# Performance work log

Measured on AMD Instinct MI355X. Metric: run time of the kernel, lower is better.

The kernel has to match this reference:

```python
import jax, jax.numpy as jnp
import numpy as np
import math

B, T, C = 2, 2048, 1024
H, DK, DV = 16, 64, 64


def setup_inputs() -> dict:
    key = jax.random.key(0)
    ks = jax.random.split(key, 5)
    # randw(*d) = randn(*d) / sqrt(d[-1])
    x = jax.random.normal(ks[0], (B, T, C), dtype=jnp.float32)
    w_q = jax.random.normal(ks[1], (H, DK, C), dtype=jnp.float32) / math.sqrt(C)
    w_k = jax.random.normal(ks[2], (H, DK, C), dtype=jnp.float32) / math.sqrt(C)
    w_v = jax.random.normal(ks[3], (H, DV, C), dtype=jnp.float32) / math.sqrt(C)
    w_o = jax.random.normal(ks[4], (H * DV, C), dtype=jnp.float32) / math.sqrt(C)
    return {"x": x, "w_q": w_q, "w_k": w_k, "w_v": w_v, "w_o": w_o}


def reference(x, w_q, w_k, w_v, w_o):
    # Full prefill: bs_q.first = 0, bs_q.nb = T, causal=True, dropout=0 (eval).
    dk = w_q.shape[1]
    q = jnp.einsum('ntc,hdc->nhtd', x, w_q)  # [B,H,T,DK]
    k = jnp.einsum('ntc,hdc->nhtd', x, w_k)  # [B,H,T,DK]
    v = jnp.einsum('ntc,hdc->nhtd', x, w_v)  # [B,H,T,DV]
    a = jnp.einsum('nhtd,nhsd->nhts', q, k) / jnp.sqrt(jnp.asarray(dk, x.dtype))
    # amm_generator: mask where query_idx < key_idx (strict upper triangle)
    t = a.shape[-1]
    mask = jnp.arange(t)[:, None] < jnp.arange(t)[None, :]  # [T,T] bool
    a = jnp.where(mask[None, None], jnp.asarray(-jnp.inf, a.dtype), a)
    a = jax.nn.softmax(a, axis=-1)
    y = jnp.einsum('nhts,nhsd->nthd', a, v)  # [B,T,H,DV]
    y = y.reshape(y.shape[0], y.shape[1], -1)  # [B,T,H*DV]
    return y @ w_o  # [B,T,C]
```

## Files before the change

kernel.cpp:

```cpp
#include <hip/hip_runtime.h>
#include <hip/hip_bf16.h>

#define B_ 2
#define T_ 2048
#define C_ 1024
#define H_ 16
#define D_ 64

typedef __attribute__((ext_vector_type(8))) short bf16x8;
typedef __attribute__((ext_vector_type(4))) float f32x4;
typedef __attribute__((ext_vector_type(8))) unsigned short u16x8;
typedef __attribute__((ext_vector_type(2))) unsigned int u32x2;
typedef __attribute__((ext_vector_type(4))) unsigned int u32x4;

__device__ __forceinline__ unsigned short bf1(float a) {
    __bf16 x = (__bf16)a;
    return __builtin_bit_cast(unsigned short, x);
}
__device__ __forceinline__ unsigned int pk2(float a, float b) {
    return (unsigned int)bf1(a) | ((unsigned int)bf1(b) << 16);
}

__device__ __forceinline__ void gll16(const void* g, void* l) {
    __builtin_amdgcn_global_load_lds(
        (const __attribute__((address_space(1))) unsigned int*)g,
        (__attribute__((address_space(3))) unsigned int*)l, 16, 0, 0);
}

__global__ __launch_bounds__(256) void prep_x(
    const float* __restrict__ x, unsigned short* __restrict__ xb)
{
    const size_t i = ((size_t)blockIdx.x * 256 + threadIdx.x) * 16;
    float4 f0 = *reinterpret_cast<const float4*>(x + i);
    float4 f1 = *reinterpret_cast<const float4*>(x + i + 4);
    float4 f2 = *reinterpret_cast<const float4*>(x + i + 8);
    float4 f3 = *reinterpret_cast<const float4*>(x + i + 12);
    u32x4 a = {pk2(f0.x, f0.y), pk2(f0.z, f0.w), pk2(f1.x, f1.y), pk2(f1.z, f1.w)};
    u32x4 b = {pk2(f2.x, f2.y), pk2(f2.z, f2.w), pk2(f3.x, f3.y), pk2(f3.z, f3.w)};
    *reinterpret_cast<u32x4*>(xb + i) = a;
    *reinterpret_cast<u32x4*>(xb + i + 8) = b;
}

__global__ __launch_bounds__(256) void prep_w(
    const float* __restrict__ wq, const float* __restrict__ wk,
    const float* __restrict__ wv, unsigned short* __restrict__ wb)
{
    const int bid = blockIdx.x, tid = threadIdx.x;
    const int rb = bid * 4;
    const float* src = (rb < 1024) ? wq + (size_t)rb * 1024
                     : (rb < 2048) ? wk + (size_t)(rb - 1024) * 1024
                                   : wv + (size_t)(rb - 2048) * 1024;
    const float sc = (rb < 1024) ? 0.125f * 1.4426950408889634f : 1.0f;
    const float4* s4 = (const float4*)src;
    u32x2* d = (u32x2*)(wb + (size_t)rb * 1024);
#pragma unroll
    for (int k = 0; k < 4; k++) {
        float4 v = s4[k * 256 + tid];
        u32x2 w;
        w[0] = pk2(v.x * sc, v.y * sc);
        w[1] = pk2(v.z * sc, v.w * sc);
        d[k * 256 + tid] = w;
    }
}

__global__ __launch_bounds__(256) void prep_wo(
    const float* __restrict__ wo, unsigned short* __restrict__ wt)
{
    __shared__ unsigned short tile[64][72];
    const int tk = (blockIdx.x & 15) << 6, tn = (blockIdx.x >> 4) << 6;
    const int r = threadIdx.x >> 2, cb = (threadIdx.x & 3) << 4;
#pragma unroll
    for (int j = 0; j < 4; j++) {
        float4 v = *reinterpret_cast<const float4*>(
            wo + (size_t)(tk + r) * 1024 + tn + cb + j * 4);
        u32x2 w;
        w[0] = pk2(v.x, v.y);
        w[1] = pk2(v.z, v.w);
        *reinterpret_cast<u32x2*>(&tile[r][cb + j * 4]) = w;
    }
    __syncthreads();
    unsigned short buf[16];
#pragma unroll
    for (int j = 0; j < 16; j++) buf[j] = tile[cb + j][r];
    unsigned short* dst = wt + (size_t)(tn + r) * 1024 + tk + cb;
    *reinterpret_cast<u16x8*>(dst) = *reinterpret_cast<u16x8*>(buf);
    *reinterpret_cast<u16x8*>(dst + 8) = *reinterpret_cast<u16x8*>(buf + 8);
}

__global__ __launch_bounds__(256) void qkv_gemm(
    const unsigned short* __restrict__ xb, const unsigned short* __restrict__ wb,
    unsigned short* __restrict__ qkv)
{
    __shared__ __align__(16) unsigned short As[2][128 * 64];
    __shared__ __align__(16) unsigned short Bs[2][128 * 64];
    const int tid = threadIdx.x;
    const int lane = tid & 63, wave = tid >> 6;
    const int g = lane >> 4, c16 = lane & 15;
    const int xcd = blockIdx.x & 7, idx = blockIdx.x >> 3;
    const int bm = (xcd << 2) + idx / 24, bn = idx % 24;
    const int jbase = bn << 7;
    const int which = jbase >> 10;

    const int srow = wave * 32 + (lane >> 3);
    const int swc = ((lane & 7) ^ (lane >> 3)) << 3;
    const unsigned short* asrc = xb + ((size_t)(bm << 7) + srow) * C_ + swc;
    const unsigned short* bsrc = wb + ((size_t)(bn << 7) + srow) * C_ + swc;

    f32x4 acc[4][4];
#pragma unroll
    for (int i = 0; i < 4; i++)
#pragma unroll
        for (int j = 0; j < 4; j++) acc[i][j] = (f32x4){0.f, 0.f, 0.f, 0.f};

    const int wm = (wave >> 1) << 6, wn = (wave & 1) << 6;

    auto stage = [&](int buf, int k0) {
#pragma unroll
        for (int i = 0; i < 4; i++) {
            gll16(asrc + k0 + i * 8 * C_, &As[buf][(wave * 32 + i * 8) << 6]);
            gll16(bsrc + k0 + i * 8 * C_, &Bs[buf][(wave * 32 + i * 8) << 6]);
        }
    };

    stage(0, 0);
    int cur = 0;
    for (int t = 0; t < 16; ++t) {
        __syncthreads();
        if (t < 15) stage(cur ^ 1, (t + 1) << 6);
#pragma unroll
        for (int kk = 0; kk < 2; kk++) {
            bf16x8 af[4], bfv[4];
#pragma unroll
            for (int m = 0; m < 4; m++)
                af[m] = *reinterpret_cast<const bf16x8*>(
                    &As[cur][((wm + m * 16 + c16) << 6) + ((((kk << 2) + g) ^ (c16 & 7)) << 3)]);
#pragma unroll
            for (int n = 0; n < 4; n++)
                bfv[n] = *reinterpret_cast<const bf16x8*>(
                    &Bs[cur][((wn + n * 16 + c16) << 6) + ((((kk << 2) + g) ^ (c16 & 7)) << 3)]);
#pragma unroll
            for (int m = 0; m < 4; m++)
#pragma unroll
                for (int n = 0; n < 4; n++)
                    acc[m][n] = __builtin_amdgcn_mfma_f32_16x16x32_bf16(af[m], bfv[n], acc[m][n], 0, 0, 0);
        }
        cur ^= 1;
    }

    if (which < 2) {
#pragma unroll
        for (int m = 0; m < 4; m++) {
            const int grow = (bm << 7) + wm + m * 16 + (g << 2);
#pragma unroll
            for (int n = 0; n < 4; n++) {
                const int jj = (jbase + wn + n * 16 + c16) & 1023;
                const int h = jj >> 6, d = jj & 63;
#pragma unroll
                for (int r = 0; r < 4; r++) {
                    const int row = grow + r;
                    const int b = row >> 11, t = row & 2047;
                    const size_t off = ((size_t)((which * B_ + b) * H_ + h) * T_ + t) * 64 + d;
                    qkv[off] = bf1(acc[m][n][r]);
                }
            }
        }
    } else {
#pragma unroll
        for (int m = 0; m < 4; m++) {
            const int grow = (bm << 7) + wm + m * 16 + (g << 2);
            const int b = grow >> 11, t = grow & 2047;
#pragma unroll
            for (int n = 0; n < 4; n++) {
                const int jj = (jbase + wn + n * 16 + c16) & 1023;
                const int h = jj >> 6, d = jj & 63;
                u32x2 w;
                w[0] = pk2(acc[m][n][0], acc[m][n][1]);
                w[1] = pk2(acc[m][n][2], acc[m][n][3]);
                const size_t off = ((size_t)((2 * B_ + b) * H_ + h) * 64 + d) * T_ + t;
                *reinterpret_cast<u32x2*>(&qkv[off]) = w;
            }
        }
    }
}

__device__ __forceinline__ void attn_tile(
    const unsigned short* __restrict__ Ks, const unsigned short* __restrict__ Vt,
    unsigned short* __restrict__ Psw,
    const bf16x8& qf0, const bf16x8& qf1,
    float& m_run, float& l_run, f32x4* acc,
    int qglob, int s0, bool diag, int g, int c16)
{
    f32x4 sfT[4];
#pragma unroll
    for (int f = 0; f < 4; f++) sfT[f] = (f32x4){0.f, 0.f, 0.f, 0.f};

    __builtin_amdgcn_s_setprio(1);
#pragma unroll
    for (int f = 0; f < 4; f++) {
        const int row = f * 16 + c16;
        const int sw = row & 7;
        bf16x8 k0 = *reinterpret_cast<const bf16x8*>(&Ks[(row << 6) + ((g ^ sw) << 3)]);
        bf16x8 k1 = *reinterpret_cast<const bf16x8*>(&Ks[(row << 6) + (((g + 4) ^ sw) << 3)]);
        sfT[f] = __builtin_amdgcn_mfma_f32_16x16x32_bf16(k0, qf0, sfT[f], 0, 0, 0);
        sfT[f] = __builtin_amdgcn_mfma_f32_16x16x32_bf16(k1, qf1, sfT[f], 0, 0, 0);
    }
    __builtin_amdgcn_s_setprio(0);

    if (diag) {
#pragma unroll
        for (int f = 0; f < 4; f++)
#pragma unroll
            for (int r = 0; r < 4; r++) {
                const int kv = s0 + f * 16 + g * 4 + r;
                if (kv > qglob) sfT[f][r] = -1e30f;
            }
    }

    float mloc = -1e30f;
#pragma unroll
    for (int f = 0; f < 4; f++)
#pragma unroll
        for (int r = 0; r < 4; r++) mloc = fmaxf(mloc, sfT[f][r]);
    mloc = fmaxf(mloc, __shfl_xor(mloc, 16, 64));
    mloc = fmaxf(mloc, __shfl_xor(mloc, 32, 64));
    const float mn = fmaxf(m_run, mloc);
    const float corr = __builtin_amdgcn_exp2f(m_run - mn);
    m_run = mn;
    float ssum = 0.f;
#pragma unroll
    for (int f = 0; f < 4; f++)
#pragma unroll
        for (int r = 0; r < 4; r++) {
            const float pv = __builtin_amdgcn_exp2f(sfT[f][r] - mn);
            sfT[f][r] = pv;
            ssum += pv;
        }
    ssum += __shfl_xor(ssum, 16, 64);
    ssum += __shfl_xor(ssum, 32, 64);
    l_run = l_run * corr + ssum;
#pragma unroll
    for (int fd = 0; fd < 4; fd++)
#pragma unroll
        for (int r = 0; r < 4; r++) acc[fd][r] *= corr;

#pragma unroll
    for (int f = 0; f < 4; f++) {
        u32x2 w;
        w[0] = pk2(sfT[f][0], sfT[f][1]);
        w[1] = pk2(sfT[f][2], sfT[f][3]);
        *reinterpret_cast<u32x2*>(&Psw[c16 * 72 + f * 16 + g * 4]) = w;
    }

    __builtin_amdgcn_s_setprio(1);
#pragma unroll
    for (int ks = 0; ks < 2; ks++) {
        bf16x8 pa = *reinterpret_cast<const bf16x8*>(&Psw[c16 * 72 + ks * 32 + (g << 3)]);
#pragma unroll
        for (int fd = 0; fd < 4; fd++) {
            const int d = fd * 16 + c16;
            bf16x8 vf = *reinterpret_cast<const bf16x8*>(
                &Vt[(d << 6) + ((((ks << 2) + g) ^ (d & 7)) << 3)]);
            acc[fd] = __builtin_amdgcn_mfma_f32_16x16x32_bf16(vf, pa, acc[fd], 0, 0, 0);
        }
    }
    __builtin_amdgcn_s_setprio(0);
}

__global__ __launch_bounds__(256) void attn(
    const unsigned short* __restrict__ qkv, unsigned short* __restrict__ y)
{
    __shared__ __align__(16) unsigned short Ks[2][64 * 64];
    __shared__ __align__(16) unsigned short Vt[2][64 * 64];
    __shared__ __align__(16) unsigned short Ps[4][16 * 72];
    const int tid = threadIdx.x, lane = tid & 63, wave = tid >> 6;
    const int g = lane >> 4, c16 = lane & 15;
    const int p = blockIdx.x & 15;
    const int bh = blockIdx.x >> 4;
    const int b = bh >> 4, h = bh & 15;
    const size_t headoff = (size_t)(b * H_ + h) * T_ * 64;
    const size_t QSZ = (size_t)B_ * H_ * T_ * 64;
    const unsigned short* qp = qkv + headoff;
    const unsigned short* kp = qkv + QSZ + headoff;
    const unsigned short* vTp = qkv + 2 * QSZ + headoff;

    const int tA = p, tB = 31 - p;
    const int qbaseA = (tA << 6) + wave * 16, qbaseB = (tB << 6) + wave * 16;

    bf16x8 qfA[2], qfB[2];
    {
        const size_t ra = (size_t)(qbaseA + c16) * 64, rb = (size_t)(qbaseB + c16) * 64;
        qfA[0] = *reinterpret_cast<const bf16x8*>(qp + ra + g * 8);
        qfA[1] = *reinterpret_cast<const bf16x8*>(qp + ra + 32 + g * 8);
        qfB[0] = *reinterpret_cast<const bf16x8*>(qp + rb + g * 8);
        qfB[1] = *reinterpret_cast<const bf16x8*>(qp + rb + 32 + g * 8);
    }

    float mA = -1e30f, lA = 0.f, mB = -1e30f, lB = 0.f;
    f32x4 accA[4], accB[4];
#pragma unroll
    for (int i = 0; i < 4; i++) {
        accA[i] = (f32x4){0.f, 0.f, 0.f, 0.f};
        accB[i] = (f32x4){0.f, 0.f, 0.f, 0.f};
    }

    const int srow8 = lane >> 3;
    const int swc = ((lane & 7) ^ srow8) << 3;
    const unsigned short* ksrc = kp + (size_t)(wave * 16 + srow8) * 64 + swc;
    const unsigned short* vsrc = vTp + (size_t)(wave * 16 + srow8) * T_ + swc;

    auto stage = [&](int buf, int s0) {
#pragma unroll
        for (int i = 0; i < 2; i++) {
            gll16(ksrc + (size_t)(s0 + i * 8) * 64, &Ks[buf][(wave * 16 + i * 8) << 6]);
            gll16(vsrc + s0 + (size_t)i * 8 * T_, &Vt[buf][(wave * 16 + i * 8) << 6]);
        }
    };

    const int nt = 32 - p;
    stage(0, 0);
    int cur = 0;
    for (int it = 0; it < nt; ++it) {
        __syncthreads();
        if (it + 1 < nt) stage(cur ^ 1, (it + 1) << 6);
        const int s0 = it << 6;

        attn_tile(Ks[cur], Vt[cur], Ps[wave], qfB[0], qfB[1], mB, lB, accB,
                  qbaseB + c16, s0, it == tB, g, c16);
        if (it <= tA)
            attn_tile(Ks[cur], Vt[cur], Ps[wave], qfA[0], qfA[1], mA, lA, accA,
                      qbaseA + c16, s0, it == tA, g, c16);
        cur ^= 1;
    }

    const float liA = 1.0f / lA, liB = 1.0f / lB;
#pragma unroll
    for (int fd = 0; fd < 4; fd++) {
        u32x2 wa, wb2;
        wa[0] = pk2(accA[fd][0] * liA, accA[fd][1] * liA);
        wa[1] = pk2(accA[fd][2] * liA, accA[fd][3] * liA);
        wb2[0] = pk2(accB[fd][0] * liB, accB[fd][1] * liB);
        wb2[1] = pk2(accB[fd][2] * liB, accB[fd][3] * liB);
        const size_t ca = ((size_t)b * T_ + qbaseA + c16) * 1024 + h * 64 + fd * 16 + g * 4;
        const size_t cb = ((size_t)b * T_ + qbaseB + c16) * 1024 + h * 64 + fd * 16 + g * 4;
        *reinterpret_cast<u32x2*>(&y[ca]) = wa;
        *reinterpret_cast<u32x2*>(&y[cb]) = wb2;
    }
}

__global__ __launch_bounds__(256) void out_proj(
    const unsigned short* __restrict__ y, const unsigned short* __restrict__ wt,
    float* __restrict__ out)
{
    __shared__ __align__(16) unsigned short As[2][128 * 64];
    __shared__ __align__(16) unsigned short Bs[2][128 * 64];
    const int tid = threadIdx.x;
    const int lane = tid & 63, wave = tid >> 6;
    const int g = lane >> 4, c16 = lane & 15;
    const int xcd = blockIdx.x & 7, idx = blockIdx.x >> 3;
    const int bm = (xcd << 2) + (idx >> 3), bn = idx & 7;
    const int wm = (wave >> 1) << 6, wn = (wave & 1) << 6;

    const int srow = wave * 32 + (lane >> 3);
    const int swc = ((lane & 7) ^ (lane >> 3)) << 3;
    const unsigned short* ysrc = y + ((size_t)(bm << 7) + srow) * 1024 + swc;
    const unsigned short* wsrc = wt + ((size_t)(bn << 7) + srow) * 1024 + swc;

    f32x4 acc[4][4];
#pragma unroll
    for (int i = 0; i < 4; i++)
#pragma unroll
        for (int j = 0; j < 4; j++) acc[i][j] = (f32x4){0.f, 0.f, 0.f, 0.f};

    auto stage = [&](int buf, int k0) {
#pragma unroll
        for (int i = 0; i < 4; i++) {
            gll16(ysrc + k0 + i * 8 * 1024, &As[buf][(wave * 32 + i * 8) << 6]);
            gll16(wsrc + k0 + i * 8 * 1024, &Bs[buf][(wave * 32 + i * 8) << 6]);
        }
    };

    stage(0, 0);
    int cur = 0;
    for (int t = 0; t < 16; ++t) {
        __syncthreads();
        if (t < 15) stage(cur ^ 1, (t + 1) << 6);
#pragma unroll
        for (int kk = 0; kk < 2; kk++) {
            bf16x8 af[4], bfr[4];
#pragma unroll
            for (int m = 0; m < 4; m++)
                af[m] = *reinterpret_cast<const bf16x8*>(
                    &As[cur][((wm + m * 16 + c16) << 6) + ((((kk << 2) + g) ^ (c16 & 7)) << 3)]);
#pragma unroll
            for (int n = 0; n < 4; n++)
                bfr[n] = *reinterpret_cast<const bf16x8*>(
                    &Bs[cur][((wn + n * 16 + c16) << 6) + ((((kk << 2) + g) ^ (c16 & 7)) << 3)]);
#pragma unroll
            for (int m = 0; m < 4; m++)
#pragma unroll
                for (int n = 0; n < 4; n++)
                    acc[m][n] = __builtin_amdgcn_mfma_f32_16x16x32_bf16(af[m], bfr[n], acc[m][n], 0, 0, 0);
        }
        cur ^= 1;
    }

#pragma unroll
    for (int m = 0; m < 4; m++) {
        const int grow = (bm << 7) + wm + m * 16 + (g << 2);
#pragma unroll
        for (int n = 0; n < 4; n++) {
            const int gcol = (bn << 7) + wn + n * 16 + c16;
#pragma unroll
            for (int r = 0; r < 4; r++)
                out[(size_t)(grow + r) * 1024 + gcol] = acc[m][n][r];
        }
    }
}

extern "C" void kernel_launch(void* const* d_in, const int* in_sizes, int n_in,
                              void* d_out, int out_size, void* d_ws, size_t ws_size,
                              hipStream_t stream) {
    const float* x  = (const float*)d_in[0];
    const float* wq = (const float*)d_in[1];
    const float* wk = (const float*)d_in[2];
    const float* wv = (const float*)d_in[3];
    const float* wo = (const float*)d_in[4];
    float* out = (float*)d_out;

    unsigned short* wb  = (unsigned short*)d_ws;
    unsigned short* y   = (unsigned short*)d_ws;
    unsigned short* qkv = (unsigned short*)d_ws + (size_t)4 * 1024 * 1024;
    unsigned short* wt  = qkv;
    unsigned short* xb  = (unsigned short*)d_out;

    prep_x<<<dim3(1024), 256, 0, stream>>>(x, xb);
    prep_w<<<dim3(768), 256, 0, stream>>>(wq, wk, wv, wb);
    qkv_gemm<<<dim3(768), 256, 0, stream>>>(xb, wb, qkv);
    attn<<<dim3(16 * B_ * H_), 256, 0, stream>>>(qkv, y);
    prep_wo<<<dim3(256), 256, 0, stream>>>(wo, wt);
    out_proj<<<dim3(256), 256, 0, stream>>>(y, wt, out);
}
```

Measured before the change: 129.9 us.

## Split paired causal query tiles into separate blocks with lazy rescaling

Attention blocks no longer pair a short and a long causal query tile. Each block now handles one 64-row query tile, and the grid is ordered longest-first, with 1024 blocks instead of 512. This aims to improve occupancy and scheduling, at the cost of K/V tiles being loaded by more blocks. It also skips the online-softmax rescale unless the running max grows by more than a threshold, and XOR-swizzles the P scratch buffer to avoid padding and bank conflicts.

```diff
diff --git a/kernel.cpp b/kernel.cpp
--- a/kernel.cpp
+++ b/kernel.cpp
@@ -183,99 +183,16 @@
     }
 }
 
-__device__ __forceinline__ void attn_tile(
-    const unsigned short* __restrict__ Ks, const unsigned short* __restrict__ Vt,
-    unsigned short* __restrict__ Psw,
-    const bf16x8& qf0, const bf16x8& qf1,
-    float& m_run, float& l_run, f32x4* acc,
-    int qglob, int s0, bool diag, int g, int c16)
-{
-    f32x4 sfT[4];
-#pragma unroll
-    for (int f = 0; f < 4; f++) sfT[f] = (f32x4){0.f, 0.f, 0.f, 0.f};
-
-    __builtin_amdgcn_s_setprio(1);
-#pragma unroll
-    for (int f = 0; f < 4; f++) {
-        const int row = f * 16 + c16;
-        const int sw = row & 7;
-        bf16x8 k0 = *reinterpret_cast<const bf16x8*>(&Ks[(row << 6) + ((g ^ sw) << 3)]);
-        bf16x8 k1 = *reinterpret_cast<const bf16x8*>(&Ks[(row << 6) + (((g + 4) ^ sw) << 3)]);
-        sfT[f] = __builtin_amdgcn_mfma_f32_16x16x32_bf16(k0, qf0, sfT[f], 0, 0, 0);
-        sfT[f] = __builtin_amdgcn_mfma_f32_16x16x32_bf16(k1, qf1, sfT[f], 0, 0, 0);
-    }
-    __builtin_amdgcn_s_setprio(0);
-
-    if (diag) {
-#pragma unroll
-        for (int f = 0; f < 4; f++)
-#pragma unroll
-            for (int r = 0; r < 4; r++) {
-                const int kv = s0 + f * 16 + g * 4 + r;
-                if (kv > qglob) sfT[f][r] = -1e30f;
-            }
-    }
-
-    float mloc = -1e30f;
-#pragma unroll
-    for (int f = 0; f < 4; f++)
-#pragma unroll
-        for (int r = 0; r < 4; r++) mloc = fmaxf(mloc, sfT[f][r]);
-    mloc = fmaxf(mloc, __shfl_xor(mloc, 16, 64));
-    mloc = fmaxf(mloc, __shfl_xor(mloc, 32, 64));
-    const float mn = fmaxf(m_run, mloc);
-    const float corr = __builtin_amdgcn_exp2f(m_run - mn);
-    m_run = mn;
-    float ssum = 0.f;
-#pragma unroll
-    for (int f = 0; f < 4; f++)
-#pragma unroll
-        for (int r = 0; r < 4; r++) {
-            const float pv = __builtin_amdgcn_exp2f(sfT[f][r] - mn);
-            sfT[f][r] = pv;
-            ssum += pv;
-        }
-    ssum += __shfl_xor(ssum, 16, 64);
-    ssum += __shfl_xor(ssum, 32, 64);
-    l_run = l_run * corr + ssum;
-#pragma unroll
-    for (int fd = 0; fd < 4; fd++)
-#pragma unroll
-        for (int r = 0; r < 4; r++) acc[fd][r] *= corr;
-
-#pragma unroll
-    for (int f = 0; f < 4; f++) {
-        u32x2 w;
-        w[0] = pk2(sfT[f][0], sfT[f][1]);
-        w[1] = pk2(sfT[f][2], sfT[f][3]);
-        *reinterpret_cast<u32x2*>(&Psw[c16 * 72 + f * 16 + g * 4]) = w;
-    }
-
-    __builtin_amdgcn_s_setprio(1);
-#pragma unroll
-    for (int ks = 0; ks < 2; ks++) {
-        bf16x8 pa = *reinterpret_cast<const bf16x8*>(&Psw[c16 * 72 + ks * 32 + (g << 3)]);
-#pragma unroll
-        for (int fd = 0; fd < 4; fd++) {
-            const int d = fd * 16 + c16;
-            bf16x8 vf = *reinterpret_cast<const bf16x8*>(
-                &Vt[(d << 6) + ((((ks << 2) + g) ^ (d & 7)) << 3)]);
-            acc[fd] = __builtin_amdgcn_mfma_f32_16x16x32_bf16(vf, pa, acc[fd], 0, 0, 0);
-        }
-    }
-    __builtin_amdgcn_s_setprio(0);
-}
-
 __global__ __launch_bounds__(256) void attn(
     const unsigned short* __restrict__ qkv, unsigned short* __restrict__ y)
 {
     __shared__ __align__(16) unsigned short Ks[2][64 * 64];
     __shared__ __align__(16) unsigned short Vt[2][64 * 64];
-    __shared__ __align__(16) unsigned short Ps[4][16 * 72];
+    __shared__ __align__(16) unsigned short Ps[4][16 * 64];
     const int tid = threadIdx.x, lane = tid & 63, wave = tid >> 6;
     const int g = lane >> 4, c16 = lane & 15;
-    const int p = blockIdx.x & 15;
-    const int bh = blockIdx.x >> 4;
+    const int qt = 31 - (blockIdx.x >> 5);
+    const int bh = blockIdx.x & 31;
     const int b = bh >> 4, h = bh & 15;
     const size_t headoff = (size_t)(b * H_ + h) * T_ * 64;
     const size_t QSZ = (size_t)B_ * H_ * T_ * 64;
@@ -283,25 +200,18 @@
     const unsigned short* kp = qkv + QSZ + headoff;
     const unsigned short* vTp = qkv + 2 * QSZ + headoff;
 
-    const int tA = p, tB = 31 - p;
-    const int qbaseA = (tA << 6) + wave * 16, qbaseB = (tB << 6) + wave * 16;
-
-    bf16x8 qfA[2], qfB[2];
+    const int qbase = (qt << 6) + wave * 16;
+    bf16x8 qf0, qf1;
     {
-        const size_t ra = (size_t)(qbaseA + c16) * 64, rb = (size_t)(qbaseB + c16) * 64;
-        qfA[0] = *reinterpret_cast<const bf16x8*>(qp + ra + g * 8);
-        qfA[1] = *reinterpret_cast<const bf16x8*>(qp + ra + 32 + g * 8);
-        qfB[0] = *reinterpret_cast<const bf16x8*>(qp + rb + g * 8);
-        qfB[1] = *reinterpret_cast<const bf16x8*>(qp + rb + 32 + g * 8);
-    }
-
-    float mA = -1e30f, lA = 0.f, mB = -1e30f, lB = 0.f;
-    f32x4 accA[4], accB[4];
-#pragma unroll
-    for (int i = 0; i < 4; i++) {
-        accA[i] = (f32x4){0.f, 0.f, 0.f, 0.f};
-        accB[i] = (f32x4){0.f, 0.f, 0.f, 0.f};
-    }
+        const size_t r0 = (size_t)(qbase + c16) * 64;
+        qf0 = *reinterpret_cast<const bf16x8*>(qp + r0 + g * 8);
+        qf1 = *reinterpret_cast<const bf16x8*>(qp + r0 + 32 + g * 8);
+    }
+
+    float m_run = -1e30f, l_run = 0.f;
+    f32x4 acc[4];
+#pragma unroll
+    for (int i = 0; i < 4; i++) acc[i] = (f32x4){0.f, 0.f, 0.f, 0.f};
 
     const int srow8 = lane >> 3;
     const int swc = ((lane & 7) ^ srow8) << 3;
@@ -316,7 +226,7 @@
         }
     };
 
-    const int nt = 32 - p;
+    const int nt = qt + 1;
     stage(0, 0);
     int cur = 0;
     for (int it = 0; it < nt; ++it) {
@@ -324,26 +234,96 @@
         if (it + 1 < nt) stage(cur ^ 1, (it + 1) << 6);
         const int s0 = it << 6;
 
-        attn_tile(Ks[cur], Vt[cur], Ps[wave], qfB[0], qfB[1], mB, lB, accB,
-                  qbaseB + c16, s0, it == tB, g, c16);
-        if (it <= tA)
-            attn_tile(Ks[cur], Vt[cur], Ps[wave], qfA[0], qfA[1], mA, lA, accA,
-                      qbaseA + c16, s0, it == tA, g, c16);
+        f32x4 sfT[4];
+#pragma unroll
+        for (int f = 0; f < 4; f++) sfT[f] = (f32x4){0.f, 0.f, 0.f, 0.f};
+        __builtin_amdgcn_s_setprio(1);
+#pragma unroll
+        for (int f = 0; f < 4; f++) {
+            const int row = f * 16 + c16;
+            const int sw = row & 7;
+            bf16x8 k0 = *reinterpret_cast<const bf16x8*>(&Ks[cur][(row << 6) + ((g ^ sw) << 3)]);
+            bf16x8 k1 = *reinterpret_cast<const bf16x8*>(&Ks[cur][(row << 6) + (((g + 4) ^ sw) << 3)]);
+            sfT[f] = __builtin_amdgcn_mfma_f32_16x16x32_bf16(k0, qf0, sfT[f], 0, 0, 0);
+            sfT[f] = __builtin_amdgcn_mfma_f32_16x16x32_bf16(k1, qf1, sfT[f], 0, 0, 0);
+        }
+        __builtin_amdgcn_s_setprio(0);
+
+        if (it == qt) {
+            const int qglob = qbase + c16;
+#pragma unroll
+            for (int f = 0; f < 4; f++)
+#pragma unroll
+                for (int r = 0; r < 4; r++) {
+                    const int kv = s0 + f * 16 + g * 4 + r;
+                    if (kv > qglob) sfT[f][r] = -1e30f;
+                }
+        }
+
+        float mloc = -1e30f;
+#pragma unroll
+        for (int f = 0; f < 4; f++)
+#pragma unroll
+            for (int r = 0; r < 4; r++) mloc = fmaxf(mloc, sfT[f][r]);
+        mloc = fmaxf(mloc, __shfl_xor(mloc, 16, 64));
+        mloc = fmaxf(mloc, __shfl_xor(mloc, 32, 64));
+        if (!__all(mloc - m_run <= 8.0f)) {
+            const float mn = fmaxf(m_run, mloc);
+            const float corr = __builtin_amdgcn_exp2f(m_run - mn);
+            m_run = mn;
+            l_run *= corr;
+#pragma unroll
+            for (int fd = 0; fd < 4; fd++)
+#pragma unroll
+                for (int r = 0; r < 4; r++) acc[fd][r] *= corr;
+        }
+        float ssum = 0.f;
+#pragma unroll
+        for (int f = 0; f < 4; f++)
+#pragma unroll
+            for (int r = 0; r < 4; r++) {
+                const float pv = __builtin_amdgcn_exp2f(sfT[f][r] - m_run);
+                sfT[f][r] = pv;
+                ssum += pv;
+            }
+        ssum += __shfl_xor(ssum, 16, 64);
+        ssum += __shfl_xor(ssum, 32, 64);
+        l_run += ssum;
+
+#pragma unroll
+        for (int f = 0; f < 4; f++) {
+            u32x2 w;
+            w[0] = pk2(sfT[f][0], sfT[f][1]);
+            w[1] = pk2(sfT[f][2], sfT[f][3]);
+            const int addr = (c16 << 6) + ((((f << 1) + (g >> 1)) ^ (c16 & 7)) << 3) + ((g & 1) << 2);
+            *reinterpret_cast<u32x2*>(&Ps[wave][addr]) = w;
+        }
+
+        __builtin_amdgcn_s_setprio(1);
+#pragma unroll
+        for (int ks = 0; ks < 2; ks++) {
+            bf16x8 pa = *reinterpret_cast<const bf16x8*>(
+                &Ps[wave][(c16 << 6) + ((((ks << 2) + g) ^ (c16 & 7)) << 3)]);
+#pragma unroll
+            for (int fd = 0; fd < 4; fd++) {
+                const int d = fd * 16 + c16;
+                bf16x8 vf = *reinterpret_cast<const bf16x8*>(
+                    &Vt[cur][(d << 6) + ((((ks << 2) + g) ^ (d & 7)) << 3)]);
+                acc[fd] = __builtin_amdgcn_mfma_f32_16x16x32_bf16(vf, pa, acc[fd], 0, 0, 0);
+            }
+        }
+        __builtin_amdgcn_s_setprio(0);
         cur ^= 1;
     }
 
-    const float liA = 1.0f / lA, liB = 1.0f / lB;
+    const float li = 1.0f / l_run;
 #pragma unroll
     for (int fd = 0; fd < 4; fd++) {
-        u32x2 wa, wb2;
-        wa[0] = pk2(accA[fd][0] * liA, accA[fd][1] * liA);
-        wa[1] = pk2(accA[fd][2] * liA, accA[fd][3] * liA);
-        wb2[0] = pk2(accB[fd][0] * liB, accB[fd][1] * liB);
-        wb2[1] = pk2(accB[fd][2] * liB, accB[fd][3] * liB);
-        const size_t ca = ((size_t)b * T_ + qbaseA + c16) * 1024 + h * 64 + fd * 16 + g * 4;
-        const size_t cb = ((size_t)b * T_ + qbaseB + c16) * 1024 + h * 64 + fd * 16 + g * 4;
-        *reinterpret_cast<u32x2*>(&y[ca]) = wa;
-        *reinterpret_cast<u32x2*>(&y[cb]) = wb2;
+        u32x2 w;
+        w[0] = pk2(acc[fd][0] * li, acc[fd][1] * li);
+        w[1] = pk2(acc[fd][2] * li, acc[fd][3] * li);
+        const size_t cy = ((size_t)b * T_ + qbase + c16) * 1024 + h * 64 + fd * 16 + g * 4;
+        *reinterpret_cast<u32x2*>(&y[cy]) = w;
     }
 }
 
@@ -436,7 +416,7 @@
     prep_x<<<dim3(1024), 256, 0, stream>>>(x, xb);
     prep_w<<<dim3(768), 256, 0, stream>>>(wq, wk, wv, wb);
     qkv_gemm<<<dim3(768), 256, 0, stream>>>(xb, wb, qkv);
-    attn<<<dim3(16 * B_ * H_), 256, 0, stream>>>(qkv, y);
+    attn<<<dim3(32 * 32), 256, 0, stream>>>(qkv, y);
     prep_wo<<<dim3(256), 256, 0, stream>>>(wo, wt);
     out_proj<<<dim3(256), 256, 0, stream>>>(y, wt, out);
 }
```

Measured after the change: 125.4 us. 3.4% less time.
